# Optimization experiments

Hardware: AMD Instinct MI355X
Metric: run time of the kernel (lower is better)

Reference implementation:

```python
import jax, jax.numpy as jnp
import numpy as np

S = 8    # number of path-segments
U = 32   # per-segment input width (subscript 'u')
V = 32   # per-segment output width (subscript 'v')
C = 32   # number of weight groups (indexed dimension)
Z = 65536  # number of rows


def setup_inputs() -> dict:
    key = jax.random.key(0)
    k1, k2, k3 = jax.random.split(key, 3)
    input1 = jax.random.normal(k1, (C, S * U * V), dtype=jnp.float32) * 0.05  # grouped weights
    input2 = jax.random.normal(k2, (Z, S * U), dtype=jnp.float32)             # row features
    counts = jnp.full((C,), Z // C, dtype=jnp.int32)                          # rows per group, contiguous
    coefficients = jax.random.uniform(k3, (S,), dtype=jnp.float32, minval=0.5, maxval=1.5)
    return {"input1": input1, "input2": input2, "counts": counts, "coefficients": coefficients}


def reference(input1, input2, counts, coefficients):
    # Segment-indexed grouped linear: rows are contiguous per group (sizes = counts).
    # For each path-segment s: out_s[z, v] = coeff_s * sum_u x_s[z, u] * W_s[g(z), u, v]
    # Final output concatenates the S segment outputs along the last dim.
    seg_ids = jnp.repeat(jnp.arange(C, dtype=jnp.int32), counts, total_repeat_length=Z)  # [Z]
    outs = []
    for s in range(S):
        W = input1[:, s * U * V:(s + 1) * U * V].reshape(C, U, V)  # [C,U,V]
        x = input2[:, s * U:(s + 1) * U]                           # [Z,U]
        Wz = W[seg_ids]                                            # [Z,U,V] gather by group
        outs.append(coefficients[s] * jnp.einsum('zu,zuv->zv', x, Wz))
    return jnp.concatenate(outs, axis=-1)  # [Z, S*V]
```

## Files before the change

### kernel.cpp

```cpp
#include <hip/hip_runtime.h>


constexpr int S = 8, U = 32, V = 32, C = 32, Z = 65536;
constexpr int SU = S * U;
constexpr int SV = S * V;
constexpr int NT = 256;
constexpr int BZ = 32;

typedef float    f4     __attribute__((ext_vector_type(4)));
typedef float    f32x16 __attribute__((ext_vector_type(16)));
typedef short    bf16x8 __attribute__((ext_vector_type(8)));
typedef unsigned u32x4  __attribute__((ext_vector_type(4)));

__device__ __forceinline__ unsigned cvtpk(float lo, float hi) {
  unsigned r;
  asm("v_cvt_pk_bf16_f32 %0, %1, %2" : "=v"(r) : "v"(lo), "v"(hi));
  return r;
}

__global__ __launch_bounds__(NT) void IndexedLinear_kernel(
    const float* __restrict__ W_all,
    const float* __restrict__ X,
    const int*   __restrict__ counts,
    const float* __restrict__ coeff,
    float*       __restrict__ out)
{
  const int tid  = threadIdx.x;
  const int lane = tid & 63;
  const int w    = tid >> 6;
  const int z0   = blockIdx.x * BZ;

  const int m  = lane & 31;
  const int h  = lane >> 5;
  const int s0 = 2 * w;

  int cnt = (lane < C) ? counts[lane] : 0;
  int inc = cnt;
  #pragma unroll
  for (int d = 1; d < 32; d <<= 1) {
    int o = __shfl_up(inc, d, 64);
    if (lane >= d) inc += o;
  }
  const int exc = inc - cnt;
  const unsigned long long ma = __ballot(lane < C && exc <= z0);
  const unsigned long long mb = __ballot(lane < C && exc <= z0 + BZ - 1);
  const int segA = __popcll(ma) - 1;
  const int segB = __popcll(mb) - 1;
  const bool uni = (segA == segB);

  if (uni) {
    const f4* Xr = (const f4*)X + (size_t)(z0 + m) * (SU / 4) + 2 * h;
    f4 xs[8];
    #pragma unroll
    for (int tt = 0; tt < 2; ++tt) {
      const int c0 = (s0 + tt) * 8;
      xs[4 * tt + 0] = Xr[c0 + 0];
      xs[4 * tt + 1] = Xr[c0 + 1];
      xs[4 * tt + 2] = Xr[c0 + 4];
      xs[4 * tt + 3] = Xr[c0 + 5];
    }

    const float* wseg = W_all + (size_t)segA * (S * U * V);
    u32x4 b1[2], b2[2];
    #pragma unroll
    for (int tt = 0; tt < 2; ++tt) {
      const int s = s0 + tt;
      const float cs = coeff[s];
      const float* wb = wseg + s * (U * V) + m;
      #pragma unroll
      for (int j = 0; j < 4; ++j) {
        b1[tt][j] = cvtpk(wb[(8 * h + 2 * j) * V] * cs,
                          wb[(8 * h + 2 * j + 1) * V] * cs);
        b2[tt][j] = cvtpk(wb[(16 + 8 * h + 2 * j) * V] * cs,
                          wb[(16 + 8 * h + 2 * j + 1) * V] * cs);
      }
    }

    #pragma unroll
    for (int tt = 0; tt < 2; ++tt) {
      const int s = s0 + tt;
      const f4 xa = xs[4 * tt + 0], xb = xs[4 * tt + 1];
      const f4 xc = xs[4 * tt + 2], xd = xs[4 * tt + 3];
      u32x4 pa, pb;
      pa[0] = cvtpk(xa[0], xa[1]); pa[1] = cvtpk(xa[2], xa[3]);
      pa[2] = cvtpk(xb[0], xb[1]); pa[3] = cvtpk(xb[2], xb[3]);
      pb[0] = cvtpk(xc[0], xc[1]); pb[1] = cvtpk(xc[2], xc[3]);
      pb[2] = cvtpk(xd[0], xd[1]); pb[3] = cvtpk(xd[2], xd[3]);
      const bf16x8 a1 = __builtin_bit_cast(bf16x8, pa);
      const bf16x8 a2 = __builtin_bit_cast(bf16x8, pb);
      f32x16 acc = {};
      acc = __builtin_amdgcn_mfma_f32_32x32x16_bf16(
          a1, __builtin_bit_cast(bf16x8, b1[tt]), acc, 0, 0, 0);
      acc = __builtin_amdgcn_mfma_f32_32x32x16_bf16(
          a2, __builtin_bit_cast(bf16x8, b2[tt]), acc, 0, 0, 0);

      float* ob = out + (size_t)z0 * SV + s * V + m;
      #pragma unroll
      for (int r = 0; r < 16; ++r) {
        const int row = (r & 3) + 8 * (r >> 2) + 4 * h;
        __builtin_nontemporal_store(acc[r], ob + (size_t)row * SV);
      }
    }
  } else {
    const int zz = z0 + m;
    int sg = 0;
    #pragma unroll 1
    for (int i = 1; i < C; ++i) {
      const int pi = __shfl(exc, i, 64);
      if (pi <= zz) sg = i;
    }
    #pragma unroll 1
    for (int tt = 0; tt < 2; ++tt) {
      const int s = s0 + tt;
      const float cs = coeff[s];
      const float* wr = W_all + (size_t)sg * (S * U * V) + s * (U * V) + 16 * h;
      float accv[16] = {};
      #pragma unroll 1
      for (int cq = 0; cq < 8; ++cq) {
        const f4 xv = ((const f4*)X)[(size_t)zz * (SU / 4) + s * 8 + cq];
        #pragma unroll
        for (int ii = 0; ii < 4; ++ii) {
          const int u = cq * 4 + ii;
          const float xu = xv[ii];
          #pragma unroll
          for (int j = 0; j < 16; ++j) accv[j] += xu * wr[u * V + j];
        }
      }
      float* ob = out + (size_t)zz * SV + s * V + 16 * h;
      #pragma unroll
      for (int j = 0; j < 16; ++j) ob[j] = accv[j] * cs;
    }
  }
}

extern "C" void kernel_launch(void* const* d_in, const int* in_sizes, int n_in,
                              void* d_out, int out_size, void* d_ws, size_t ws_size,
                              hipStream_t stream) {
  const float* input1       = (const float*)d_in[0];
  const float* input2       = (const float*)d_in[1];
  const int*   counts       = (const int*)d_in[2];
  const float* coefficients = (const float*)d_in[3];
  float*       out          = (float*)d_out;

  const int grid = Z / BZ;
  IndexedLinear_kernel<<<grid, NT, 0, stream>>>(input1, input2, counts,
                                                coefficients, out);
}
```

Before: 120.7 us.

## Process four row tiles per block with double-buffered X prefetch and cached weights

Each block now handles four consecutive 32-row tiles instead of one. While the current tile is computed, the X rows for the next tile are prefetched into a second register buffer, and the converted bf16 weight fragments are reloaded only when the group changes. This is meant to hide load latency and cut redundant weight loads and conversions, at the cost of more registers, a four-times smaller grid, and less parallelism. An unused f2bf helper is also added.

```diff
diff --git a/kernel.cpp b/kernel.cpp
--- a/kernel.cpp
+++ b/kernel.cpp
@@ -6,6 +6,7 @@
 constexpr int SV = S * V;
 constexpr int NT = 256;
 constexpr int BZ = 32;
+constexpr int TPB = 4;
 
 typedef float    f4     __attribute__((ext_vector_type(4)));
 typedef float    f32x16 __attribute__((ext_vector_type(16)));
@@ -18,6 +19,21 @@
   return r;
 }
 
+__device__ __forceinline__ short f2bf(float f) {
+  unsigned u = __builtin_bit_cast(unsigned, f);
+  u = (u + 0x7FFFu + ((u >> 16) & 1u)) >> 16;
+  return (short)u;
+}
+
+#define LOADX(dst, zt)                                                        \
+  do {                                                                        \
+    const f4* Xr_ = (const f4*)X + (size_t)((zt) + m) * (SU / 4) + 2 * h;     \
+    dst[0] = Xr_[c0 + 0];  dst[1] = Xr_[c0 + 1];                              \
+    dst[2] = Xr_[c0 + 4];  dst[3] = Xr_[c0 + 5];                              \
+    dst[4] = Xr_[c0 + 8];  dst[5] = Xr_[c0 + 9];                              \
+    dst[6] = Xr_[c0 + 12]; dst[7] = Xr_[c0 + 13];                             \
+  } while (0)
+
 __global__ __launch_bounds__(NT) void IndexedLinear_kernel(
     const float* __restrict__ W_all,
     const float* __restrict__ X,
@@ -28,11 +44,15 @@
   const int tid  = threadIdx.x;
   const int lane = tid & 63;
   const int w    = tid >> 6;
-  const int z0   = blockIdx.x * BZ;
+  const int zb   = blockIdx.x * (BZ * TPB);
 
   const int m  = lane & 31;
   const int h  = lane >> 5;
   const int s0 = 2 * w;
+  const int c0 = s0 * 8;
+
+  f4 xA[8], xB[8];
+  LOADX(xA, zb);
 
   int cnt = (lane < C) ? counts[lane] : 0;
   int inc = cnt;
@@ -42,93 +62,97 @@
     if (lane >= d) inc += o;
   }
   const int exc = inc - cnt;
-  const unsigned long long ma = __ballot(lane < C && exc <= z0);
-  const unsigned long long mb = __ballot(lane < C && exc <= z0 + BZ - 1);
-  const int segA = __popcll(ma) - 1;
-  const int segB = __popcll(mb) - 1;
-  const bool uni = (segA == segB);
 
-  if (uni) {
-    const f4* Xr = (const f4*)X + (size_t)(z0 + m) * (SU / 4) + 2 * h;
-    f4 xs[8];
-    #pragma unroll
-    for (int tt = 0; tt < 2; ++tt) {
-      const int c0 = (s0 + tt) * 8;
-      xs[4 * tt + 0] = Xr[c0 + 0];
-      xs[4 * tt + 1] = Xr[c0 + 1];
-      xs[4 * tt + 2] = Xr[c0 + 4];
-      xs[4 * tt + 3] = Xr[c0 + 5];
-    }
+  int curseg = -1;
+  u32x4 b1[2], b2[2];
 
-    const float* wseg = W_all + (size_t)segA * (S * U * V);
-    u32x4 b1[2], b2[2];
-    #pragma unroll
-    for (int tt = 0; tt < 2; ++tt) {
-      const int s = s0 + tt;
-      const float cs = coeff[s];
-      const float* wb = wseg + s * (U * V) + m;
-      #pragma unroll
-      for (int j = 0; j < 4; ++j) {
-        b1[tt][j] = cvtpk(wb[(8 * h + 2 * j) * V] * cs,
-                          wb[(8 * h + 2 * j + 1) * V] * cs);
-        b2[tt][j] = cvtpk(wb[(16 + 8 * h + 2 * j) * V] * cs,
-                          wb[(16 + 8 * h + 2 * j + 1) * V] * cs);
-      }
-    }
+  #pragma unroll
+  for (int t = 0; t < TPB; ++t) {
+    f4* cur = (t & 1) ? xB : xA;
+    f4* nxt = (t & 1) ? xA : xB;
+    const int z0 = zb + t * BZ;
 
-    #pragma unroll
-    for (int tt = 0; tt < 2; ++tt) {
-      const int s = s0 + tt;
-      const f4 xa = xs[4 * tt + 0], xb = xs[4 * tt + 1];
-      const f4 xc = xs[4 * tt + 2], xd = xs[4 * tt + 3];
-      u32x4 pa, pb;
-      pa[0] = cvtpk(xa[0], xa[1]); pa[1] = cvtpk(xa[2], xa[3]);
-      pa[2] = cvtpk(xb[0], xb[1]); pa[3] = cvtpk(xb[2], xb[3]);
-      pb[0] = cvtpk(xc[0], xc[1]); pb[1] = cvtpk(xc[2], xc[3]);
-      pb[2] = cvtpk(xd[0], xd[1]); pb[3] = cvtpk(xd[2], xd[3]);
-      const bf16x8 a1 = __builtin_bit_cast(bf16x8, pa);
-      const bf16x8 a2 = __builtin_bit_cast(bf16x8, pb);
-      f32x16 acc = {};
-      acc = __builtin_amdgcn_mfma_f32_32x32x16_bf16(
-          a1, __builtin_bit_cast(bf16x8, b1[tt]), acc, 0, 0, 0);
-      acc = __builtin_amdgcn_mfma_f32_32x32x16_bf16(
-          a2, __builtin_bit_cast(bf16x8, b2[tt]), acc, 0, 0, 0);
+    if (t + 1 < TPB) LOADX(nxt, z0 + BZ);
 
-      float* ob = out + (size_t)z0 * SV + s * V + m;
-      #pragma unroll
-      for (int r = 0; r < 16; ++r) {
-        const int row = (r & 3) + 8 * (r >> 2) + 4 * h;
-        __builtin_nontemporal_store(acc[r], ob + (size_t)row * SV);
-      }
-    }
-  } else {
-    const int zz = z0 + m;
-    int sg = 0;
-    #pragma unroll 1
-    for (int i = 1; i < C; ++i) {
-      const int pi = __shfl(exc, i, 64);
-      if (pi <= zz) sg = i;
-    }
-    #pragma unroll 1
-    for (int tt = 0; tt < 2; ++tt) {
-      const int s = s0 + tt;
-      const float cs = coeff[s];
-      const float* wr = W_all + (size_t)sg * (S * U * V) + s * (U * V) + 16 * h;
-      float accv[16] = {};
-      #pragma unroll 1
-      for (int cq = 0; cq < 8; ++cq) {
-        const f4 xv = ((const f4*)X)[(size_t)zz * (SU / 4) + s * 8 + cq];
+    const unsigned long long ma = __ballot(lane < C && exc <= z0);
+    const unsigned long long mb = __ballot(lane < C && exc <= z0 + BZ - 1);
+    const int segA = __popcll(ma) - 1;
+    const int segB = __popcll(mb) - 1;
+    const bool uni = (segA == segB);
+
+    if (uni) {
+      if (segA != curseg) {
+        curseg = segA;
+        const float* wseg = W_all + (size_t)segA * (S * U * V);
         #pragma unroll
-        for (int ii = 0; ii < 4; ++ii) {
-          const int u = cq * 4 + ii;
-          const float xu = xv[ii];
+        for (int tt = 0; tt < 2; ++tt) {
+          const int s = s0 + tt;
+          const float cs = coeff[s];
+          const float* wb = wseg + s * (U * V) + m;
           #pragma unroll
-          for (int j = 0; j < 16; ++j) accv[j] += xu * wr[u * V + j];
+          for (int j = 0; j < 4; ++j) {
+            b1[tt][j] = cvtpk(wb[(8 * h + 2 * j) * V] * cs,
+                              wb[(8 * h + 2 * j + 1) * V] * cs);
+            b2[tt][j] = cvtpk(wb[(16 + 8 * h + 2 * j) * V] * cs,
+                              wb[(16 + 8 * h + 2 * j + 1) * V] * cs);
+          }
         }
       }
-      float* ob = out + (size_t)zz * SV + s * V + 16 * h;
+
       #pragma unroll
-      for (int j = 0; j < 16; ++j) ob[j] = accv[j] * cs;
+      for (int tt = 0; tt < 2; ++tt) {
+        const int s = s0 + tt;
+        const f4 xa = cur[4 * tt + 0], xb = cur[4 * tt + 1];
+        const f4 xc = cur[4 * tt + 2], xd = cur[4 * tt + 3];
+        u32x4 pa, pb;
+        pa[0] = cvtpk(xa[0], xa[1]); pa[1] = cvtpk(xa[2], xa[3]);
+        pa[2] = cvtpk(xb[0], xb[1]); pa[3] = cvtpk(xb[2], xb[3]);
+        pb[0] = cvtpk(xc[0], xc[1]); pb[1] = cvtpk(xc[2], xc[3]);
+        pb[2] = cvtpk(xd[0], xd[1]); pb[3] = cvtpk(xd[2], xd[3]);
+        const bf16x8 a1 = __builtin_bit_cast(bf16x8, pa);
+        const bf16x8 a2 = __builtin_bit_cast(bf16x8, pb);
+        f32x16 acc = {};
+        acc = __builtin_amdgcn_mfma_f32_32x32x16_bf16(
+            a1, __builtin_bit_cast(bf16x8, b1[tt]), acc, 0, 0, 0);
+        acc = __builtin_amdgcn_mfma_f32_32x32x16_bf16(
+            a2, __builtin_bit_cast(bf16x8, b2[tt]), acc, 0, 0, 0);
+
+        float* ob = out + (size_t)z0 * SV + s * V + m;
+        #pragma unroll
+        for (int r = 0; r < 16; ++r) {
+          const int row = (r & 3) + 8 * (r >> 2) + 4 * h;
+          __builtin_nontemporal_store(acc[r], ob + (size_t)row * SV);
+        }
+      }
+    } else {
+      const int zz = z0 + m;
+      int sg = 0;
+      #pragma unroll 1
+      for (int i = 1; i < C; ++i) {
+        const int pi = __shfl(exc, i, 64);
+        if (pi <= zz) sg = i;
+      }
+      #pragma unroll 1
+      for (int tt = 0; tt < 2; ++tt) {
+        const int s = s0 + tt;
+        const float cs = coeff[s];
+        const float* wr = W_all + (size_t)sg * (S * U * V) + s * (U * V) + 16 * h;
+        float accv[16] = {};
+        #pragma unroll 1
+        for (int cq = 0; cq < 8; ++cq) {
+          const f4 xv = ((const f4*)X)[(size_t)zz * (SU / 4) + s * 8 + cq];
+          #pragma unroll
+          for (int ii = 0; ii < 4; ++ii) {
+            const int u = cq * 4 + ii;
+            const float xu = xv[ii];
+            #pragma unroll
+            for (int j = 0; j < 16; ++j) accv[j] += xu * wr[u * V + j];
+          }
+        }
+        float* ob = out + (size_t)zz * SV + s * V + 16 * h;
+        #pragma unroll
+        for (int j = 0; j < 16; ++j) ob[j] = accv[j] * cs;
+      }
     }
   }
 }
@@ -142,7 +166,7 @@
   const float* coefficients = (const float*)d_in[3];
   float*       out          = (float*)d_out;
 
-  const int grid = Z / BZ;
+  const int grid = Z / (BZ * TPB);
   IndexedLinear_kernel<<<grid, NT, 0, stream>>>(input1, input2, counts,
                                                 coefficients, out);
 }
```

After: 119.1 us. About the same (-1.4%).
